# Kernel tuning notes

Hardware: AMD Instinct MI355X
Metric: run time of the kernel (lower is better)

## Reference

```python
import jax, jax.numpy as jnp
import numpy as np
from jax import lax

V, E, H, B, T = 50000, 512, 512, 128, 256
OUT = 2

def gru(x, Wi, Wh, bi, bh):
    # x: [B,T,D]; PyTorch GRU equations, h0 = 0. Returns all hidden states [B,T,H].
    Bsz = x.shape[0]
    Hd = Wh.shape[1]
    xW = jnp.einsum('btd,gd->btg', x, Wi) + bi  # [B,T,3H], precompute input projections
    def step(h, xw):
        gh = h @ Wh.T + bh
        xr, xz, xn = jnp.split(xw, 3, axis=-1)
        hr, hz, hn = jnp.split(gh, 3, axis=-1)
        r = jax.nn.sigmoid(xr + hr)
        z = jax.nn.sigmoid(xz + hz)
        n = jnp.tanh(xn + r * hn)
        h_new = (1.0 - z) * n + z * h
        return h_new, h_new
    h0 = jnp.zeros((Bsz, Hd), x.dtype)
    _, hs = lax.scan(step, h0, jnp.swapaxes(xW, 0, 1))
    return jnp.swapaxes(hs, 0, 1)

def dual_attention(u, r, u_all_sum, Aw, bw, Ww):
    # u, r: [B,T,D] (query side / response side per timestep, vectorized over T).
    # w_t[b,t] = (u A^T + b) . r  (the original bmm of [B,1,D] x [B,D,1])
    w = jnp.einsum('btd,btd->bt', jnp.einsum('btd,ed->bte', u, Aw) + bw, r)
    # score = softmax over D of tanh(w) * Ww  (Linear(1, D, bias=False))
    sc = jax.nn.softmax(jnp.tanh(w)[..., None] * Ww[None, None, :], axis=-1)  # [B,T,D]
    # sum_s embed[b,s,:] * score[b,t,:] = score * (sum over time) ; then * r_t
    return sc * u_all_sum[:, None, :] * r  # [B,T,D]

def setup_inputs() -> dict:
    key = jax.random.key(0)
    ks = jax.random.split(key, 24)
    d = {}
    d['ask'] = jax.random.randint(ks[0], (B, T), 0, V, dtype=jnp.int32)
    d['answer'] = jax.random.randint(ks[1], (B, T), 0, V, dtype=jnp.int32)
    d['ask_keyword'] = jax.random.randint(ks[2], (B, T), 0, V, dtype=jnp.int32)
    d['answer_keyword'] = jax.random.randint(ks[3], (B, T), 0, V, dtype=jnp.int32)
    d['embed'] = jax.random.normal(ks[4], (V, E), jnp.float32) * 0.02
    # GRU 1: input E -> hidden H
    d['Wi1'] = jax.random.normal(ks[5], (3 * H, E), jnp.float32) * 0.05
    d['Wh1'] = jax.random.normal(ks[6], (3 * H, H), jnp.float32) * 0.05
    d['bi1'] = jnp.zeros((3 * H,), jnp.float32)
    d['bh1'] = jnp.zeros((3 * H,), jnp.float32)
    # word attention: Linear(E,E) + Linear(1,E,bias=False)
    d['Aw'] = jax.random.normal(ks[7], (E, E), jnp.float32) * 0.05
    d['bw'] = jnp.zeros((E,), jnp.float32)
    d['Ww'] = jax.random.normal(ks[8], (E,), jnp.float32) * 0.05
    # seq attention: Linear(H,H) + Linear(1,H,bias=False)
    d['As'] = jax.random.normal(ks[9], (H, H), jnp.float32) * 0.05
    d['bs'] = jnp.zeros((H,), jnp.float32)
    d['Ws'] = jax.random.normal(ks[10], (H,), jnp.float32) * 0.05
    # GRU 2: input E+H -> hidden H
    d['Wi2'] = jax.random.normal(ks[11], (3 * H, E + H), jnp.float32) * 0.05
    d['Wh2'] = jax.random.normal(ks[12], (3 * H, H), jnp.float32) * 0.05
    d['bi2'] = jnp.zeros((3 * H,), jnp.float32)
    d['bh2'] = jnp.zeros((3 * H,), jnp.float32)
    # final classifier
    d['Wf'] = jax.random.normal(ks[13], (OUT, H), jnp.float32) * 0.05
    d['bf'] = jnp.zeros((OUT,), jnp.float32)
    return d

def reference(ask, answer, ask_keyword, answer_keyword, embed, Wi1, Wh1, bi1, bh1,
              Aw, bw, Ww, As, bs, Ws, Wi2, Wh2, bi2, bh2, Wf, bf):
    ask_e = embed[ask]            # [B,T,E]
    ans_e = embed[answer]
    ask_kw = embed[ask_keyword]
    ans_kw = embed[answer_keyword]
    h_ask = gru(ask_e, Wi1, Wh1, bi1, bh1)  # [B,T,H]
    h_ans = gru(ans_e, Wi1, Wh1, bi1, bh1)
    # dual attention, vectorized over the original Python loop over t
    ctx_word = dual_attention(ask_kw, ans_kw, ask_kw.sum(axis=1), Aw, bw, Ww)   # [B,T,E]
    ctx_seq = dual_attention(h_ask, h_ans, h_ask.sum(axis=1), As, bs, Ws)       # [B,T,H]
    v = jnp.concatenate([ctx_word, ctx_seq], axis=-1)  # [B,T,E+H]
    h2 = gru(v, Wi2, Wh2, bi2, bh2)[:, -1, :]  # final hidden state [B,H]
    # dropout is identity in eval mode
    return jax.nn.softmax(h2 @ Wf.T + bf, axis=1)
```

## Files before the change

kernel.cpp:

```cpp
#include <hip/hip_runtime.h>
#include <cstdio>

typedef __bf16 bf16x8 __attribute__((ext_vector_type(8)));
typedef float f32x4 __attribute__((ext_vector_type(4)));

#define DEV __device__ __forceinline__

DEV short f2bf(float f) {
    unsigned u = __builtin_bit_cast(unsigned, f);
    u += 0x7fffu + ((u >> 16) & 1u);
    return (short)(u >> 16);
}
DEV float bf2f(short s) {
    unsigned u = ((unsigned)(unsigned short)s) << 16;
    return __builtin_bit_cast(float, u);
}
DEV float sigmoidf_(float x) { return 1.0f / (1.0f + __expf(-x)); }
DEV float tanhf_(float x) { float e = __expf(2.0f * x); return 1.0f - 2.0f / (e + 1.0f); }

DEV void gload_lds16(const void* g, void* l) {
    __builtin_amdgcn_global_load_lds(
        (__attribute__((address_space(1))) void*)(g),
        (__attribute__((address_space(3))) void*)(l), 16, 0, 0);
}

DEV f32x4 mfma16(bf16x8 a, bf16x8 b, f32x4 c) {
    return __builtin_amdgcn_mfma_f32_16x16x32_bf16(a, b, c, 0, 0, 0);
}

__global__ void f2bf_vec(const float* __restrict__ in, short* __restrict__ out, int n4) {
    int i = blockIdx.x * 256 + threadIdx.x;
    if (i >= n4) return;
    float4 v = reinterpret_cast<const float4*>(in)[i];
    short4 o;
    o.x = f2bf(v.x); o.y = f2bf(v.y); o.z = f2bf(v.z); o.w = f2bf(v.w);
    reinterpret_cast<short4*>(out)[i] = o;
}

__global__ void pack_wh(const float* __restrict__ Wh, short* __restrict__ Wp) {
    int tile = blockIdx.x, kk = blockIdx.y, l = threadIdx.x;
    int n = tile * 16 + (l & 15);
    int k0 = kk * 32 + (l >> 4) * 8;
    const float* src = Wh + (size_t)n * 512 + k0;
    short o[8];
#pragma unroll
    for (int e = 0; e < 8; e++) o[e] = f2bf(src[e]);
    *(int4*)(Wp + ((size_t)(tile * 16 + kk) * 64 + l) * 8) = *(int4*)o;
}

enum { M_XW1 = 0, M_UAW = 1, M_UAS = 2, M_XW2 = 3 };

template<int MODE>
__global__ __launch_bounds__(256) void gemm_bt(
    const short* __restrict__ Abase, const short* __restrict__ A2,
    const int* __restrict__ tok0, const int* __restrict__ tok1,
    const short* __restrict__ W, const float* __restrict__ bias,
    short* __restrict__ C, int M, int N, int K)
{
    __shared__ short Als[128 * 64];
    __shared__ short Bls[128 * 64];
    int tid = threadIdx.x;
    int m0 = blockIdx.y * 128, n0 = blockIdx.x * 128;
    int kc = (tid & 7) * 8;

    const short* arow[4];
#pragma unroll
    for (int i = 0; i < 4; i++) {
        int gm = m0 + i * 32 + (tid >> 3);
        if (MODE == M_XW1) {
            int t = gm >> 8, s = gm & 255;
            int tok = (s < 128) ? tok0[s * 256 + t] : tok1[(s - 128) * 256 + t];
            arow[i] = Abase + (size_t)tok * 512;
        } else if (MODE == M_UAW) {
            int t = gm >> 7, b = gm & 127;
            arow[i] = Abase + (size_t)tok0[b * 256 + t] * 512;
        } else if (MODE == M_UAS) {
            int t = gm >> 7, b = gm & 127;
            arow[i] = Abase + ((size_t)t * 256 + b) * 512;
        } else {
            arow[i] = Abase + (size_t)gm * 512;
        }
    }

    f32x4 acc[4][4] = {};
    int l = tid & 63, w = tid >> 6;
    int wm = (w >> 1) * 64, wn = (w & 1) * 64;

    for (int kt = 0; kt < K; kt += 64) {
#pragma unroll
        for (int i = 0; i < 4; i++) {
            const short* asrc;
            if (MODE == M_XW2) {
                int gm = m0 + i * 32 + (tid >> 3);
                const short* base = (kt < 512) ? Abase : A2;
                asrc = base + (size_t)gm * 512 + (kt & 511) + kc;
            } else {
                asrc = arow[i] + kt + kc;
            }
            gload_lds16(asrc, &Als[i * 2048 + tid * 8]);
        }
#pragma unroll
        for (int i = 0; i < 4; i++) {
            const short* bsrc = W + (size_t)(n0 + i * 32 + (tid >> 3)) * K + kt + kc;
            gload_lds16(bsrc, &Bls[i * 2048 + tid * 8]);
        }
        __syncthreads();
#pragma unroll
        for (int kk = 0; kk < 2; kk++) {
            int ko = kk * 32 + (l >> 4) * 8;
            bf16x8 af[4], bfr[4];
#pragma unroll
            for (int mi = 0; mi < 4; mi++)
                af[mi] = *(const bf16x8*)&Als[(wm + mi * 16 + (l & 15)) * 64 + ko];
#pragma unroll
            for (int ni = 0; ni < 4; ni++)
                bfr[ni] = *(const bf16x8*)&Bls[(wn + ni * 16 + (l & 15)) * 64 + ko];
#pragma unroll
            for (int mi = 0; mi < 4; mi++)
#pragma unroll
                for (int ni = 0; ni < 4; ni++)
                    acc[mi][ni] = mfma16(af[mi], bfr[ni], acc[mi][ni]);
        }
        __syncthreads();
    }
#pragma unroll
    for (int ni = 0; ni < 4; ni++) {
        int col = n0 + wn + ni * 16 + (l & 15);
        float bv = bias[col];
#pragma unroll
        for (int mi = 0; mi < 4; mi++) {
            int row0 = m0 + wm + mi * 16 + (l >> 4) * 4;
#pragma unroll
            for (int j = 0; j < 4; j++)
                C[(size_t)(row0 + j) * N + col] = f2bf(acc[mi][ni][j] + bv);
        }
    }
}

template<int WRITE_ALL>
__global__ __launch_bounds__(256, 1) void gru_scan10(
    const short* __restrict__ xW,
    const short* __restrict__ Wp,
    const float* __restrict__ bh,
    short* __restrict__ hb0, short* __restrict__ hb1,
    short* __restrict__ h_all,
    float* __restrict__ h_final,
    unsigned* __restrict__ done,
    int S, int T)
{
    __shared__ char wl[96 * 1024];
    __shared__ char sl[32 * 1024];
    __shared__ char ho[2048];

    int cb = blockIdx.x;
    int rg = blockIdx.y;
    int r0 = rg * 32;
    int tid = threadIdx.x;
    int w = tid >> 6, l = tid & 63;
    int rt = w >> 1, ct = w & 1;
    int lrow = l & 15, lq = l >> 4;
    int colg = cb * 32 + ct * 16 + lrow;
    unsigned* mydone = done + rg * 32;

    for (int rr = 0; rr < 24; rr++) {
        int flat = rr * 256 + tid;
        int lane = flat & 63, kk = (flat >> 6) & 15, lg = flat >> 10;
        int g = lg >> 1, c2 = lg & 1;
        gload_lds16(Wp + (((size_t)(g * 32 + cb * 2 + c2) * 16 + kk) * 64 + lane) * 8,
                    wl + flat * 16);
    }
    float bhv[3];
#pragma unroll
    for (int g = 0; g < 3; g++) bhv[g] = bh[g * 512 + colg];
    __syncthreads();

    float hp[4] = {};

    for (int t = 0; t < T; t++) {
        short xrv[4], xzv[4], xnv[4];
        const short* xbase = xW + ((size_t)t * S + r0) * 1536 + colg;
#pragma unroll
        for (int j = 0; j < 4; j++) {
            const short* xp = xbase + (size_t)(rt * 16 + lq * 4 + j) * 1536;
            xrv[j] = xp[0]; xzv[j] = xp[512]; xnv[j] = xp[1024];
        }

        f32x4 acc[3] = {};
        if (t > 0) {
            const short* hprev = ((t & 1) ? hb0 : hb1) + (size_t)r0 * 512;
            if (tid < 16) {
                while (__hip_atomic_load(&mydone[tid], __ATOMIC_RELAXED,
                                         __HIP_MEMORY_SCOPE_AGENT) < (unsigned)t)
                    __builtin_amdgcn_s_sleep(1);
            }
            __syncthreads();
            unsigned long long v[16];
            const unsigned long long* sp = (const unsigned long long*)hprev;
#pragma unroll
            for (int k = 0; k < 16; k++)
                v[k] = __hip_atomic_load(sp + k * 256 + tid,
                                         __ATOMIC_RELAXED, __HIP_MEMORY_SCOPE_AGENT);
#pragma unroll
            for (int k = 0; k < 16; k++) {
                int off = (k * 256 + tid) * 8;
                int row = off >> 10, colb = off & 1023;
                *(unsigned long long*)(sl + row * 1024 + (colb ^ ((row & 7) << 4))) = v[k];
            }
            __syncthreads();
            bf16x8 afr[16];
            int ar = rt * 16 + lrow;
#pragma unroll
            for (int kk = 0; kk < 16; kk++) {
                int colb = kk * 64 + lq * 16;
                afr[kk] = *(const bf16x8*)(sl + ar * 1024 + (colb ^ ((ar & 7) << 4)));
            }
#pragma unroll
            for (int g = 0; g < 3; g++) {
                const char* bbase = wl + (size_t)((g * 2 + ct) * 16) * 1024 + l * 16;
#pragma unroll
                for (int kk = 0; kk < 16; kk++) {
                    bf16x8 bfr = *(const bf16x8*)(bbase + kk * 1024);
                    acc[g] = mfma16(afr[kk], bfr, acc[g]);
                }
            }
        }

        float hv[4];
#pragma unroll
        for (int j = 0; j < 4; j++) {
            float r = sigmoidf_(bf2f(xrv[j]) + bhv[0] + acc[0][j]);
            float z = sigmoidf_(bf2f(xzv[j]) + bhv[1] + acc[1][j]);
            float n = tanhf_(bf2f(xnv[j]) + r * (acc[2][j] + bhv[2]));
            hv[j] = (1.f - z) * n + z * hp[j];
            hp[j] = hv[j];
            *(short*)(ho + (rt * 16 + lq * 4 + j) * 64 + (ct * 16 + lrow) * 2) = f2bf(hv[j]);
        }
        __syncthreads();
        {
            int row = tid >> 3, ch = tid & 7;
            unsigned long long val = *(const unsigned long long*)(ho + row * 64 + ch * 8);
            short* hnew = (t & 1) ? hb1 : hb0;
            __hip_atomic_store(
                (unsigned long long*)(hnew + (size_t)(r0 + row) * 512 + cb * 32 + ch * 4),
                val, __ATOMIC_RELAXED, __HIP_MEMORY_SCOPE_AGENT);
            if (WRITE_ALL)
                *(unsigned long long*)(h_all + ((size_t)t * S + r0 + row) * 512 + cb * 32 + ch * 4) = val;
        }
        if (!WRITE_ALL && t == T - 1) {
#pragma unroll
            for (int j = 0; j < 4; j++)
                h_final[(size_t)(r0 + rt * 16 + lq * 4 + j) * 512 + colg] = hv[j];
        }
        __syncthreads();
        if (tid == 0)
            __hip_atomic_store(&mydone[cb], (unsigned)(t + 1),
                               __ATOMIC_RELAXED, __HIP_MEMORY_SCOPE_AGENT);
    }
}

__global__ void embed_sum_k(const short* __restrict__ ebf, const int* __restrict__ tok,
                            float* __restrict__ out) {
    int b = blockIdx.x, d = threadIdx.x;
    float a0 = 0.f, a1 = 0.f;
    for (int t = 0; t < 256; t++) {
        const short* row = ebf + (size_t)tok[b * 256 + t] * 512;
        a0 += bf2f(row[d]); a1 += bf2f(row[d + 256]);
    }
    out[b * 512 + d] = a0; out[b * 512 + d + 256] = a1;
}
__global__ void hall_sum_k(const short* __restrict__ h_all, float* __restrict__ out) {
    int b = blockIdx.x, d = threadIdx.x;
    float a0 = 0.f, a1 = 0.f;
    for (int t = 0; t < 256; t++) {
        const short* row = h_all + ((size_t)t * 256 + b) * 512;
        a0 += bf2f(row[d]); a1 += bf2f(row[d + 256]);
    }
    out[b * 512 + d] = a0; out[b * 512 + d + 256] = a1;
}

template<int WORD>
__global__ __launch_bounds__(256) void attn_combine(
    const short* __restrict__ uA, const short* __restrict__ rsrc,
    const int* __restrict__ rtok, const float* __restrict__ usum,
    const float* __restrict__ Wv, short* __restrict__ ctx)
{
    int l = threadIdx.x & 63, w = threadIdx.x >> 6;
    int m = blockIdx.x * 4 + w;
    int t = m >> 7, b = m & 127;
    const short* rrow;
    if (WORD) rrow = rsrc + (size_t)rtok[b * 256 + t] * 512;
    else      rrow = rsrc + ((size_t)t * 256 + 128 + b) * 512;
    const short* urow = uA + (size_t)m * 512;
    int d0 = l * 8;
    short ru[8], uu[8];
    *(int4*)ru = *(const int4*)(rrow + d0);
    *(int4*)uu = *(const int4*)(urow + d0);
    float rv[8], dot = 0.f;
#pragma unroll
    for (int i = 0; i < 8; i++) { rv[i] = bf2f(ru[i]); dot += rv[i] * bf2f(uu[i]); }
#pragma unroll
    for (int off = 32; off >= 1; off >>= 1) dot += __shfl_xor(dot, off);
    float tw = tanhf_(dot);
    float e[8], se = 0.f;
#pragma unroll
    for (int i = 0; i < 8; i++) { e[i] = __expf(tw * Wv[d0 + i]); se += e[i]; }
#pragma unroll
    for (int off = 32; off >= 1; off >>= 1) se += __shfl_xor(se, off);
    float inv = 1.f / se;
    short ov[8];
#pragma unroll
    for (int i = 0; i < 8; i++) ov[i] = f2bf(e[i] * inv * usum[b * 512 + d0 + i] * rv[i]);
    *(int4*)(ctx + (size_t)m * 512 + d0) = *(int4*)ov;
}

__global__ void final_head_k(const float* __restrict__ h2, const float* __restrict__ Wf,
                             const float* __restrict__ bfv, float* __restrict__ out) {
    int b = blockIdx.x, l = threadIdx.x;
    float d0 = 0.f, d1 = 0.f;
    for (int k = l; k < 512; k += 64) {
        float h = h2[b * 512 + k];
        d0 += h * Wf[k];
        d1 += h * Wf[512 + k];
    }
#pragma unroll
    for (int off = 32; off >= 1; off >>= 1) { d0 += __shfl_xor(d0, off); d1 += __shfl_xor(d1, off); }
    if (l == 0) {
        float l0 = d0 + bfv[0], l1 = d1 + bfv[1];
        float mx = fmaxf(l0, l1);
        float e0 = __expf(l0 - mx), e1 = __expf(l1 - mx);
        float s = e0 + e1;
        out[b * 2] = e0 / s; out[b * 2 + 1] = e1 / s;
    }
}

extern "C" void kernel_launch(void* const* d_in, const int* in_sizes, int n_in,
                              void* d_out, int out_size, void* d_ws, size_t ws_size,
                              hipStream_t stream)
{
    const int* ask    = (const int*)d_in[0];
    const int* answer = (const int*)d_in[1];
    const int* askkw  = (const int*)d_in[2];
    const int* anskw  = (const int*)d_in[3];
    const float* embed = (const float*)d_in[4];
    const float* Wi1 = (const float*)d_in[5];
    const float* Wh1 = (const float*)d_in[6];
    const float* bi1 = (const float*)d_in[7];
    const float* bh1 = (const float*)d_in[8];
    const float* Aw  = (const float*)d_in[9];
    const float* bw  = (const float*)d_in[10];
    const float* Ww  = (const float*)d_in[11];
    const float* As  = (const float*)d_in[12];
    const float* bs  = (const float*)d_in[13];
    const float* Ws  = (const float*)d_in[14];
    const float* Wi2 = (const float*)d_in[15];
    const float* Wh2 = (const float*)d_in[16];
    const float* bi2 = (const float*)d_in[17];
    const float* bh2 = (const float*)d_in[18];
    const float* Wf  = (const float*)d_in[19];
    const float* bfv = (const float*)d_in[20];

    char* ws = (char*)d_ws;
    size_t off = 0;
    auto alloc = [&](size_t bytes) -> void* {
        void* p = (void*)(ws + off);
        off += (bytes + 255) & ~(size_t)255;
        return p;
    };
    short* embed_bf = (short*)alloc(50000ULL * 512 * 2);
    short* Wi1b = (short*)alloc(1536 * 512 * 2);
    short* Wp1  = (short*)alloc(1536 * 512 * 2);
    short* Awb  = (short*)alloc(512 * 512 * 2);
    short* Asb  = (short*)alloc(512 * 512 * 2);
    short* Wi2b = (short*)alloc(1536 * 1024 * 2);
    short* Wp2  = (short*)alloc(1536 * 512 * 2);
    char* X = (char*)alloc(201326592ULL);
    short* xW1  = (short*)X;
    short* uA   = (short*)X;
    short* ctxW = (short*)(X + 33554432);
    short* ctxS = (short*)(X + 67108864);
    short* xW2  = (short*)(X + 100663296);
    short* h_all = (short*)alloc(256ULL * 256 * 512 * 2);
    short* hb0 = (short*)alloc(256 * 512 * 2);
    short* hb1 = (short*)alloc(256 * 512 * 2);
    float* usumW = (float*)alloc(128 * 512 * 4);
    float* usumS = (float*)alloc(128 * 512 * 4);
    float* h2f   = (float*)alloc(128 * 512 * 4);
    unsigned* done1 = (unsigned*)alloc(8 * 32 * 4);
    unsigned* done2 = (unsigned*)alloc(4 * 32 * 4);

    if (off > ws_size) {
        fprintf(stderr, "kernel_launch: workspace too small: need %zu have %zu\n", off, ws_size);
        return;
    }

    hipMemsetAsync(done1, 0, 8 * 32 * 4, stream);
    hipMemsetAsync(done2, 0, 4 * 32 * 4, stream);

    auto cv = [&](const float* src, short* dst, int n) {
        int n4 = n / 4;
        f2bf_vec<<<(n4 + 255) / 256, 256, 0, stream>>>(src, dst, n4);
    };
    cv(embed, embed_bf, 50000 * 512);
    cv(Wi1, Wi1b, 1536 * 512);
    cv(Aw, Awb, 512 * 512);
    cv(As, Asb, 512 * 512);
    cv(Wi2, Wi2b, 1536 * 1024);
    pack_wh<<<dim3(96, 16), 64, 0, stream>>>(Wh1, Wp1);
    pack_wh<<<dim3(96, 16), 64, 0, stream>>>(Wh2, Wp2);

    gemm_bt<M_XW1><<<dim3(12, 512), 256, 0, stream>>>(
        embed_bf, nullptr, ask, answer, Wi1b, bi1, xW1, 65536, 1536, 512);

    {
        const short* xWa = xW1; const short* Wpa = Wp1; const float* bha = bh1;
        short* a0 = hb0; short* a1 = hb1; short* ha = h_all; float* hf = h2f;
        unsigned* dp = done1; int S = 256, T = 256;
        void* args[] = { (void*)&xWa, (void*)&Wpa, (void*)&bha, (void*)&a0, (void*)&a1,
                         (void*)&ha, (void*)&hf, (void*)&dp, (void*)&S, (void*)&T };
        hipError_t e = hipLaunchCooperativeKernel(
            reinterpret_cast<void*>(&gru_scan10<1>), dim3(16, 8), dim3(256), args, 0, stream);
        if (e != hipSuccess)
            gru_scan10<1><<<dim3(16, 8), 256, 0, stream>>>(xWa, Wpa, bha, a0, a1, ha, hf, dp, S, T);
    }

    embed_sum_k<<<128, 256, 0, stream>>>(embed_bf, askkw, usumW);
    gemm_bt<M_UAW><<<dim3(4, 256), 256, 0, stream>>>(
        embed_bf, nullptr, askkw, nullptr, Awb, bw, uA, 32768, 512, 512);
    attn_combine<1><<<8192, 256, 0, stream>>>(uA, embed_bf, anskw, usumW, Ww, ctxW);

    hall_sum_k<<<128, 256, 0, stream>>>(h_all, usumS);
    gemm_bt<M_UAS><<<dim3(4, 256), 256, 0, stream>>>(
        h_all, nullptr, nullptr, nullptr, Asb, bs, uA, 32768, 512, 512);
    attn_combine<0><<<8192, 256, 0, stream>>>(uA, h_all, nullptr, usumS, Ws, ctxS);

    gemm_bt<M_XW2><<<dim3(12, 256), 256, 0, stream>>>(
        ctxW, ctxS, nullptr, nullptr, Wi2b, bi2, xW2, 32768, 1536, 1024);

    {
        const short* xWa = xW2; const short* Wpa = Wp2; const float* bha = bh2;
        short* a0 = hb0; short* a1 = hb1; short* ha = nullptr; float* hf = h2f;
        unsigned* dp = done2; int S = 128, T = 256;
        void* args[] = { (void*)&xWa, (void*)&Wpa, (void*)&bha, (void*)&a0, (void*)&a1,
                         (void*)&ha, (void*)&hf, (void*)&dp, (void*)&S, (void*)&T };
        hipError_t e = hipLaunchCooperativeKernel(
            reinterpret_cast<void*>(&gru_scan10<0>), dim3(16, 4), dim3(256), args, 0, stream);
        if (e != hipSuccess)
            gru_scan10<0><<<dim3(16, 4), 256, 0, stream>>>(xWa, Wpa, bha, a0, a1, ha, hf, dp, S, T);
    }

    final_head_k<<<128, 64, 0, stream>>>(h2f, Wf, bfv, (float*)d_out);
}
```

Measured before the change: 2.227 ms.

## Fuse input-projection GEMM into GRU scan kernel with producer/consumer blocks

The separate xW GEMM launches before each GRU scan are removed. Extra producer blocks in the same cooperative launch now compute the input projections timestep-slice by timestep-slice and publish per-slice counters, which scan blocks poll before consuming a timestep. The intent is to overlap the GEMM with the latency-bound recurrence and drop a kernel boundary. The risks are producer blocks contending for CUs and bandwidth, and reliance on all 256 blocks being co-resident, since the spin-waits deadlock otherwise. The LDS row stride of the h output staging buffer is also padded from 64 to 72 bytes, likely to reduce bank conflicts.

```diff
diff --git a/kernel.cpp b/kernel.cpp
--- a/kernel.cpp
+++ b/kernel.cpp
@@ -26,6 +26,10 @@
 
 DEV f32x4 mfma16(bf16x8 a, bf16x8 b, f32x4 c) {
     return __builtin_amdgcn_mfma_f32_16x16x32_bf16(a, b, c, 0, 0, 0);
+}
+
+DEV unsigned ald(const unsigned* p) {
+    return __hip_atomic_load(p, __ATOMIC_RELAXED, __HIP_MEMORY_SCOPE_AGENT);
 }
 
 __global__ void f2bf_vec(const float* __restrict__ in, short* __restrict__ out, int n4) {
@@ -67,18 +71,12 @@
 #pragma unroll
     for (int i = 0; i < 4; i++) {
         int gm = m0 + i * 32 + (tid >> 3);
-        if (MODE == M_XW1) {
-            int t = gm >> 8, s = gm & 255;
-            int tok = (s < 128) ? tok0[s * 256 + t] : tok1[(s - 128) * 256 + t];
-            arow[i] = Abase + (size_t)tok * 512;
-        } else if (MODE == M_UAW) {
+        if (MODE == M_UAW) {
             int t = gm >> 7, b = gm & 127;
             arow[i] = Abase + (size_t)tok0[b * 256 + t] * 512;
-        } else if (MODE == M_UAS) {
+        } else {
             int t = gm >> 7, b = gm & 127;
             arow[i] = Abase + ((size_t)t * 256 + b) * 512;
-        } else {
-            arow[i] = Abase + (size_t)gm * 512;
         }
     }
 
@@ -88,22 +86,12 @@
 
     for (int kt = 0; kt < K; kt += 64) {
 #pragma unroll
-        for (int i = 0; i < 4; i++) {
-            const short* asrc;
-            if (MODE == M_XW2) {
-                int gm = m0 + i * 32 + (tid >> 3);
-                const short* base = (kt < 512) ? Abase : A2;
-                asrc = base + (size_t)gm * 512 + (kt & 511) + kc;
-            } else {
-                asrc = arow[i] + kt + kc;
-            }
-            gload_lds16(asrc, &Als[i * 2048 + tid * 8]);
-        }
-#pragma unroll
-        for (int i = 0; i < 4; i++) {
-            const short* bsrc = W + (size_t)(n0 + i * 32 + (tid >> 3)) * K + kt + kc;
-            gload_lds16(bsrc, &Bls[i * 2048 + tid * 8]);
-        }
+        for (int i = 0; i < 4; i++)
+            gload_lds16(arow[i] + kt + kc, &Als[i * 2048 + tid * 8]);
+#pragma unroll
+        for (int i = 0; i < 4; i++)
+            gload_lds16(W + (size_t)(n0 + i * 32 + (tid >> 3)) * K + kt + kc,
+                        &Bls[i * 2048 + tid * 8]);
         __syncthreads();
 #pragma unroll
         for (int kk = 0; kk < 2; kk++) {
@@ -137,25 +125,129 @@
     }
 }
 
-template<int WRITE_ALL>
-__global__ __launch_bounds__(256, 1) void gru_scan10(
-    const short* __restrict__ xW,
-    const short* __restrict__ Wp,
-    const float* __restrict__ bh,
+template<int MODE>
+DEV void produce(char* smem, int pid, int nprod, int nslices, int tps,
+                 const short* Abase, const short* A2,
+                 const int* tok0, const int* tok1,
+                 const short* W, const float* bias, short* C,
+                 int N, int K, unsigned* slice_cnt)
+{
+    short* Als = (short*)smem;
+    short* Bls = (short*)(smem + 16384);
+    short* Ct  = (short*)(smem + 32768);
+    int tid = threadIdx.x;
+    int l = tid & 63, w = tid >> 6;
+    int wm = (w >> 1) * 64, wn = (w & 1) * 64;
+    int kc = (tid & 7) * 8;
+    int ntile = nslices * tps;
+
+    for (int q = pid; q < ntile; q += nprod) {
+        int slice = q / tps, j = q % tps;
+        int m0 = (MODE == M_XW1) ? (slice * 2 + (j >= 12 ? 1 : 0)) * 128 : slice * 128;
+        int n0 = (MODE == M_XW1) ? (j % 12) * 128 : j * 128;
+
+        const short* arow[4];
+#pragma unroll
+        for (int i = 0; i < 4; i++) {
+            int gm = m0 + i * 32 + (tid >> 3);
+            if (MODE == M_XW1) {
+                int t = gm >> 8, s = gm & 255;
+                int tok = (s < 128) ? tok0[s * 256 + t] : tok1[(s - 128) * 256 + t];
+                arow[i] = Abase + (size_t)tok * 512;
+            } else {
+                arow[i] = Abase + (size_t)gm * 512;
+            }
+        }
+
+        f32x4 acc[4][4] = {};
+        for (int kt = 0; kt < K; kt += 64) {
+#pragma unroll
+            for (int i = 0; i < 4; i++) {
+                const short* asrc;
+                if (MODE == M_XW2) {
+                    int gm = m0 + i * 32 + (tid >> 3);
+                    const short* base = (kt < 512) ? Abase : A2;
+                    asrc = base + (size_t)gm * 512 + (kt & 511) + kc;
+                } else {
+                    asrc = arow[i] + kt + kc;
+                }
+                gload_lds16(asrc, Als + i * 2048 + tid * 8);
+            }
+#pragma unroll
+            for (int i = 0; i < 4; i++)
+                gload_lds16(W + (size_t)(n0 + i * 32 + (tid >> 3)) * K + kt + kc,
+                            Bls + i * 2048 + tid * 8);
+            __syncthreads();
+#pragma unroll
+            for (int kk = 0; kk < 2; kk++) {
+                int ko = kk * 32 + (l >> 4) * 8;
+                bf16x8 af[4], bfr[4];
+#pragma unroll
+                for (int mi = 0; mi < 4; mi++)
+                    af[mi] = *(const bf16x8*)&Als[(wm + mi * 16 + (l & 15)) * 64 + ko];
+#pragma unroll
+                for (int ni = 0; ni < 4; ni++)
+                    bfr[ni] = *(const bf16x8*)&Bls[(wn + ni * 16 + (l & 15)) * 64 + ko];
+#pragma unroll
+                for (int mi = 0; mi < 4; mi++)
+#pragma unroll
+                    for (int ni = 0; ni < 4; ni++)
+                        acc[mi][ni] = mfma16(af[mi], bfr[ni], acc[mi][ni]);
+            }
+            __syncthreads();
+        }
+#pragma unroll
+        for (int ni = 0; ni < 4; ni++) {
+            float bv = bias[n0 + wn + ni * 16 + (l & 15)];
+#pragma unroll
+            for (int mi = 0; mi < 4; mi++)
+#pragma unroll
+                for (int jj = 0; jj < 4; jj++)
+                    Ct[(wm + mi * 16 + (l >> 4) * 4 + jj) * 128 + wn + ni * 16 + (l & 15)] =
+                        f2bf(acc[mi][ni][jj] + bv);
+        }
+        __syncthreads();
+        for (int r = 0; r < 16; r++) {
+            int idx = r * 256 + tid;
+            int row = idx >> 5, cc = idx & 31;
+            unsigned long long val = *(const unsigned long long*)(Ct + row * 128 + cc * 4);
+            __hip_atomic_store((unsigned long long*)(C + (size_t)(m0 + row) * N + n0 + cc * 4),
+                               val, __ATOMIC_RELAXED, __HIP_MEMORY_SCOPE_AGENT);
+        }
+        __syncthreads();
+        if (tid == 0)
+            __hip_atomic_fetch_add(&slice_cnt[slice], 1u,
+                                   __ATOMIC_RELAXED, __HIP_MEMORY_SCOPE_AGENT);
+    }
+}
+
+template<int WRITE_ALL, int MODE>
+__global__ __launch_bounds__(256, 1) void gru_fused(
+    const short* xW, const short* __restrict__ Wp, const float* __restrict__ bh,
     short* __restrict__ hb0, short* __restrict__ hb1,
-    short* __restrict__ h_all,
-    float* __restrict__ h_final,
-    unsigned* __restrict__ done,
-    int S, int T)
+    short* __restrict__ h_all, float* __restrict__ h_final,
+    unsigned* __restrict__ done, unsigned* __restrict__ slice_cnt,
+    const short* __restrict__ Abase, const short* __restrict__ A2,
+    const int* __restrict__ tok0, const int* __restrict__ tok1,
+    const short* __restrict__ W, const float* __restrict__ bias, short* C,
+    int S, int T, int NSCAN, int nprod, int tps, int N, int K)
 {
-    __shared__ char wl[96 * 1024];
-    __shared__ char sl[32 * 1024];
-    __shared__ char ho[2048];
-
-    int cb = blockIdx.x;
-    int rg = blockIdx.y;
+    __shared__ char smem[133376];
+    int bid = blockIdx.x;
+    int tid = threadIdx.x;
+
+    if (bid >= NSCAN) {
+        produce<MODE>(smem, bid - NSCAN, nprod, T, tps,
+                      Abase, A2, tok0, tok1, W, bias, C, N, K, slice_cnt);
+        return;
+    }
+
+    char* wl = smem;
+    char* sl = smem + 98304;
+    char* ho = smem + 131072;
+
+    int cb = bid & 15, rg = bid >> 4;
     int r0 = rg * 32;
-    int tid = threadIdx.x;
     int w = tid >> 6, l = tid & 63;
     int rt = w >> 1, ct = w & 1;
     int lrow = l & 15, lq = l >> 4;
@@ -177,6 +269,14 @@
     float hp[4] = {};
 
     for (int t = 0; t < T; t++) {
+        if (tid < 16) {
+            if (t > 0)
+                while (ald(&mydone[tid]) < (unsigned)t) __builtin_amdgcn_s_sleep(1);
+        } else if (tid == 16) {
+            while (ald(&slice_cnt[t]) < (unsigned)tps) __builtin_amdgcn_s_sleep(1);
+        }
+        __syncthreads();
+
         short xrv[4], xzv[4], xnv[4];
         const short* xbase = xW + ((size_t)t * S + r0) * 1536 + colg;
 #pragma unroll
@@ -188,12 +288,6 @@
         f32x4 acc[3] = {};
         if (t > 0) {
             const short* hprev = ((t & 1) ? hb0 : hb1) + (size_t)r0 * 512;
-            if (tid < 16) {
-                while (__hip_atomic_load(&mydone[tid], __ATOMIC_RELAXED,
-                                         __HIP_MEMORY_SCOPE_AGENT) < (unsigned)t)
-                    __builtin_amdgcn_s_sleep(1);
-            }
-            __syncthreads();
             unsigned long long v[16];
             const unsigned long long* sp = (const unsigned long long*)hprev;
 #pragma unroll
@@ -233,12 +327,12 @@
             float n = tanhf_(bf2f(xnv[j]) + r * (acc[2][j] + bhv[2]));
             hv[j] = (1.f - z) * n + z * hp[j];
             hp[j] = hv[j];
-            *(short*)(ho + (rt * 16 + lq * 4 + j) * 64 + (ct * 16 + lrow) * 2) = f2bf(hv[j]);
+            *(short*)(ho + (rt * 16 + lq * 4 + j) * 72 + (ct * 16 + lrow) * 2) = f2bf(hv[j]);
         }
         __syncthreads();
         {
             int row = tid >> 3, ch = tid & 7;
-            unsigned long long val = *(const unsigned long long*)(ho + row * 64 + ch * 8);
+            unsigned long long val = *(const unsigned long long*)(ho + row * 72 + ch * 8);
             short* hnew = (t & 1) ? hb1 : hb0;
             __hip_atomic_store(
                 (unsigned long long*)(hnew + (size_t)(r0 + row) * 512 + cb * 32 + ch * 4),
@@ -387,6 +481,8 @@
     float* h2f   = (float*)alloc(128 * 512 * 4);
     unsigned* done1 = (unsigned*)alloc(8 * 32 * 4);
     unsigned* done2 = (unsigned*)alloc(4 * 32 * 4);
+    unsigned* slc1  = (unsigned*)alloc(256 * 4);
+    unsigned* slc2  = (unsigned*)alloc(256 * 4);
 
     if (off > ws_size) {
         fprintf(stderr, "kernel_launch: workspace too small: need %zu have %zu\n", off, ws_size);
@@ -395,6 +491,8 @@
 
     hipMemsetAsync(done1, 0, 8 * 32 * 4, stream);
     hipMemsetAsync(done2, 0, 4 * 32 * 4, stream);
+    hipMemsetAsync(slc1, 0, 256 * 4, stream);
+    hipMemsetAsync(slc2, 0, 256 * 4, stream);
 
     auto cv = [&](const float* src, short* dst, int n) {
         int n4 = n / 4;
@@ -408,19 +506,26 @@
     pack_wh<<<dim3(96, 16), 64, 0, stream>>>(Wh1, Wp1);
     pack_wh<<<dim3(96, 16), 64, 0, stream>>>(Wh2, Wp2);
 
-    gemm_bt<M_XW1><<<dim3(12, 512), 256, 0, stream>>>(
-        embed_bf, nullptr, ask, answer, Wi1b, bi1, xW1, 65536, 1536, 512);
-
     {
         const short* xWa = xW1; const short* Wpa = Wp1; const float* bha = bh1;
         short* a0 = hb0; short* a1 = hb1; short* ha = h_all; float* hf = h2f;
-        unsigned* dp = done1; int S = 256, T = 256;
+        unsigned* dp = done1; unsigned* sc = slc1;
+        const short* Ab = embed_bf; const short* A2p = nullptr;
+        const int* t0 = ask; const int* t1 = answer;
+        const short* Wm = Wi1b; const float* bi = bi1; short* Cp = xW1;
+        int S = 256, T = 256, NSCAN = 128, nprod = 128, tps = 24, N = 1536, K = 512;
         void* args[] = { (void*)&xWa, (void*)&Wpa, (void*)&bha, (void*)&a0, (void*)&a1,
-                         (void*)&ha, (void*)&hf, (void*)&dp, (void*)&S, (void*)&T };
+                         (void*)&ha, (void*)&hf, (void*)&dp, (void*)&sc,
+                         (void*)&Ab, (void*)&A2p, (void*)&t0, (void*)&t1,
+                         (void*)&Wm, (void*)&bi, (void*)&Cp,
+                         (void*)&S, (void*)&T, (void*)&NSCAN, (void*)&nprod,
+                         (void*)&tps, (void*)&N, (void*)&K };
         hipError_t e = hipLaunchCooperativeKernel(
-            reinterpret_cast<void*>(&gru_scan10<1>), dim3(16, 8), dim3(256), args, 0, stream);
+            reinterpret_cast<void*>(&gru_fused<1, M_XW1>), dim3(256), dim3(256), args, 0, stream);
         if (e != hipSuccess)
-            gru_scan10<1><<<dim3(16, 8), 256, 0, stream>>>(xWa, Wpa, bha, a0, a1, ha, hf, dp, S, T);
+            gru_fused<1, M_XW1><<<256, 256, 0, stream>>>(
+                xWa, Wpa, bha, a0, a1, ha, hf, dp, sc, Ab, A2p, t0, t1, Wm, bi, Cp,
+                S, T, NSCAN, nprod, tps, N, K);
     }
 
     embed_sum_k<<<128, 256, 0, stream>>>(embed_bf, askkw, usumW);
@@ -433,19 +538,26 @@
         h_all, nullptr, nullptr, nullptr, Asb, bs, uA, 32768, 512, 512);
     attn_combine<0><<<8192, 256, 0, stream>>>(uA, h_all, nullptr, usumS, Ws, ctxS);
 
-    gemm_bt<M_XW2><<<dim3(12, 256), 256, 0, stream>>>(
-        ctxW, ctxS, nullptr, nullptr, Wi2b, bi2, xW2, 32768, 1536, 1024);
-
     {
         const short* xWa = xW2; const short* Wpa = Wp2; const float* bha = bh2;
         short* a0 = hb0; short* a1 = hb1; short* ha = nullptr; float* hf = h2f;
-        unsigned* dp = done2; int S = 128, T = 256;
+        unsigned* dp = done2; unsigned* sc = slc2;
+        const short* Ab = ctxW; const short* A2p = ctxS;
+        const int* t0 = nullptr; const int* t1 = nullptr;
+        const short* Wm = Wi2b; const float* bi = bi2; short* Cp = xW2;
+        int S = 128, T = 256, NSCAN = 64, nprod = 192, tps = 12, N = 1536, K = 1024;
         void* args[] = { (void*)&xWa, (void*)&Wpa, (void*)&bha, (void*)&a0, (void*)&a1,
-                         (void*)&ha, (void*)&hf, (void*)&dp, (void*)&S, (void*)&T };
+                         (void*)&ha, (void*)&hf, (void*)&dp, (void*)&sc,
+                         (void*)&Ab, (void*)&A2p, (void*)&t0, (void*)&t1,
+                         (void*)&Wm, (void*)&bi, (void*)&Cp,
+                         (void*)&S, (void*)&T, (void*)&NSCAN, (void*)&nprod,
+                         (void*)&tps, (void*)&N, (void*)&K };
         hipError_t e = hipLaunchCooperativeKernel(
-            reinterpret_cast<void*>(&gru_scan10<0>), dim3(16, 4), dim3(256), args, 0, stream);
+            reinterpret_cast<void*>(&gru_fused<0, M_XW2>), dim3(256), dim3(256), args, 0, stream);
         if (e != hipSuccess)
-            gru_scan10<0><<<dim3(16, 4), 256, 0, stream>>>(xWa, Wpa, bha, a0, a1, ha, hf, dp, S, T);
+            gru_fused<0, M_XW2><<<256, 256, 0, stream>>>(
+                xWa, Wpa, bha, a0, a1, ha, hf, dp, sc, Ab, A2p, t0, t1, Wm, bi, Cp,
+                S, T, NSCAN, nprod, tps, N, K);
     }
 
     final_head_k<<<128, 64, 0, stream>>>(h2f, Wf, bfv, (float*)d_out);
```

After: 1.977 ms. -11.2%, faster.
